# Kernel tuning notes

Measured on AMD Instinct MI355X. Metric: run time of the kernel, lower is better.

The kernel has to match this reference:

```python
import jax, jax.numpy as jnp
import numpy as np

B, N, T, D = 4, 256, 64, 128
DR, DH = 32, 128  # d_relation, d_hidden


def setup_inputs() -> dict:
    key = jax.random.key(0)
    ks = jax.random.split(key, 12)
    s = 0.05
    return {
        "H": jax.random.normal(ks[0], (B, N, T, D), jnp.float32),
        "R": jax.random.normal(ks[1], (B, N, N, DR), jnp.float32),
        "delta_H": jax.random.normal(ks[2], (B, N, T, D), jnp.float32),
        # params (torch Linear convention: W @ x + b with W shape (out, in))
        "Wq": jax.random.normal(ks[3], (DH, D), jnp.float32) * s,
        "bq": jnp.zeros((DH,), jnp.float32),
        "Wk": jax.random.normal(ks[4], (DH, D), jnp.float32) * s,
        "bk": jnp.zeros((DH,), jnp.float32),
        "Wr": jax.random.normal(ks[5], (DH, DR), jnp.float32) * s,
        "br": jnp.zeros((DH,), jnp.float32),
        "Wf": jax.random.normal(ks[6], (D, 3 * D + DR), jnp.float32) * s,
        "bf": jnp.zeros((D,), jnp.float32),
        "gamma": jnp.ones((D,), jnp.float32),
        "beta": jnp.zeros((D,), jnp.float32),
    }


def reference(H, R, delta_H, Wq, bq, Wk, bk, Wr, br, Wf, bf, gamma, beta):
    Bm, Nn, Tt, Dd = H.shape
    dr = R.shape[-1]

    # projections (eval mode: dropout is identity)
    q = jnp.einsum('bitd,hd->bith', H, Wq) + bq           # (B,N,T,DH)
    k = jnp.einsum('bjtd,hd->bjth', H, Wk) + bk           # (B,N,T,DH)
    rproj = jnp.einsum('bijr,hr->bijh', R, Wr) + br       # (B,N,N,DH)

    # attn_score[b,i,j,t] = <q_i[t], k_j[t] + Wr(r_ij)> / sqrt(d_model)
    scores = (jnp.einsum('bith,bjth->bijt', q, k)
              + jnp.einsum('bith,bijh->bijt', q, rproj)) / jnp.sqrt(jnp.asarray(Dd, H.dtype))
    w = jax.nn.softmax(scores, axis=-1)                   # softmax over time t
    # exclude the j == i pair (original loop skips it)
    w = w * (1.0 - jnp.eye(Nn, dtype=w.dtype))[None, :, :, None]

    # fuse Linear decomposed over the concat [h_i, h_j, r_ij, sum_t delta_h_j]
    W1 = Wf[:, :Dd]                 # acts on h_i
    W2 = Wf[:, Dd:2 * Dd]           # acts on h_j
    W3 = Wf[:, 2 * Dd:2 * Dd + dr]  # acts on r_ij
    W4 = Wf[:, 2 * Dd + dr:]        # acts on delta sum

    A = jnp.einsum('bitd,ed->bite', H, W1)                       # (B,N,T,D)
    Bj = jnp.einsum('bjtd,ed->bjte', H, W2)                      # (B,N,T,D)
    Cij = jnp.einsum('bijr,er->bije', R, W3)                     # (B,N,N,D)
    Ej = jnp.einsum('bjd,ed->bje', delta_H.sum(axis=2), W4)      # (B,N,D)

    wsum = w.sum(axis=2)                                         # (B,N,T)
    z = ((A + bf) * wsum[..., None]
         + jnp.einsum('bijt,bjte->bite', w, Bj)
         + jnp.einsum('bijt,bije->bite', w, Cij)
         + jnp.einsum('bijt,bje->bite', w, Ej))

    # residual + LayerNorm over last dim
    x = H + z
    mu = x.mean(axis=-1, keepdims=True)
    var = x.var(axis=-1, keepdims=True)
    return (x - mu) / jnp.sqrt(var + 1e-5) * gamma + beta
```

## Files before the change

kernel.cpp:

```cpp
#include <hip/hip_runtime.h>

typedef __attribute__((ext_vector_type(4))) float f32x4;
typedef __attribute__((ext_vector_type(8))) short short8;

constexpr int NB = 4, NS = 256, NT = 64, ND = 128, NR = 32;
constexpr int WFR = 3 * ND + NR;
constexpr float SCALE = 0.08838834764831845f;

__device__ __forceinline__ unsigned short f2bf(float f) {
  unsigned x = __float_as_uint(f);
  return (unsigned short)((x + 0x7FFFu + ((x >> 16) & 1u)) >> 16);
}
__device__ __forceinline__ float bf2f(unsigned short u) {
  return __uint_as_float((unsigned)u << 16);
}

__global__ __launch_bounds__(256) void kPrep(
    const float* __restrict__ Wq, const float* __restrict__ Wk,
    const float* __restrict__ Wr, const float* __restrict__ br,
    const float* __restrict__ bq, const float* __restrict__ Wf,
    const float* __restrict__ dH, const float* __restrict__ R,
    unsigned short* __restrict__ Wqb, unsigned short* __restrict__ Wkb,
    unsigned short* __restrict__ W1b, unsigned short* __restrict__ W2b,
    unsigned short* __restrict__ W3b, unsigned short* __restrict__ Wqrt,
    float* __restrict__ Gbias, unsigned short* __restrict__ Ejt,
    unsigned short* __restrict__ Rb, unsigned short* __restrict__ Rtb) {
  __shared__ __align__(16) char smem[17408];
  const int blk = blockIdx.x, tid = threadIdx.x;
  if (blk < 116) {
    if (blk < 64) {
      const int which = blk >> 4;
      const int idx = ((blk & 15) * 256 + tid) * 4;
      const int e = idx >> 7, d = idx & 127;
      float4 v;
      unsigned short* dst;
      if (which == 0)      { v = *(const float4*)&Wq[idx];            dst = Wqb; }
      else if (which == 1) { v = *(const float4*)&Wk[idx];            dst = Wkb; }
      else if (which == 2) { v = *(const float4*)&Wf[e * WFR + d];        dst = W1b; }
      else                 { v = *(const float4*)&Wf[e * WFR + ND + d];   dst = W2b; }
      dst[idx + 0] = f2bf(v.x); dst[idx + 1] = f2bf(v.y);
      dst[idx + 2] = f2bf(v.z); dst[idx + 3] = f2bf(v.w);
    } else if (blk < 68) {
      const int idx = ((blk - 64) * 256 + tid) * 4;
      const int e = idx >> 5, r = idx & 31;
      float4 v = *(const float4*)&Wf[e * WFR + 2 * ND + r];
      W3b[idx + 0] = f2bf(v.x); W3b[idx + 1] = f2bf(v.y);
      W3b[idx + 2] = f2bf(v.z); W3b[idx + 3] = f2bf(v.w);
    } else {
      const int rr = blk - 68;
      float* Vl = (float*)smem;
      float* gbl = Vl + 128;
      if (tid < 128) {
        float v = 0.f;
        if (rr < 32) v = Wr[tid * 32 + rr];
        else if (rr == 32) v = br[tid];
        Vl[tid] = v;
        gbl[tid] = bq[tid] * v;
      }
      __syncthreads();
      if (tid < 128) {
        float acc = 0.f;
        #pragma unroll 8
        for (int h = 0; h < 128; ++h) acc += Wq[h * 128 + tid] * Vl[h];
        Wqrt[rr * 128 + tid] = f2bf(acc * SCALE);
      }
      if (tid == 0) {
        float g = 0.f;
        for (int h = 0; h < 128; ++h) g += gbl[h];
        Gbias[rr] = g * SCALE;
      }
    }
  } else if (blk < 628) {
    float* ds = (float*)smem;
    const int half = tid >> 7, d = tid & 127;
    const int bj = (blk - 116) * 2 + half;
    const int b = bj >> 8, j = bj & 255;
    const float* p = dH + (size_t)bj * NT * ND + d;
    float s = 0.f;
    #pragma unroll 8
    for (int t = 0; t < NT; ++t) s += p[t * ND];
    ds[half * 128 + d] = s;
    __syncthreads();
    const float* w4 = Wf + (size_t)d * WFR + 2 * ND + NR;
    float acc = 0.f;
    #pragma unroll 8
    for (int dd = 0; dd < ND; ++dd) acc += ds[half * 128 + dd] * w4[dd];
    Ejt[((size_t)b * 128 + d) * 256 + j] = f2bf(acc);
  } else {
    unsigned short* rt = (unsigned short*)smem;
    const int bi = blk - 628;
    const float* src = R + (size_t)bi * 8192;
    #pragma unroll
    for (int it = 0; it < 8; ++it) {
      const int idx = (tid + it * 256) * 4;
      const float4 v = *(const float4*)&src[idx];
      const unsigned short s0 = f2bf(v.x), s1 = f2bf(v.y);
      const unsigned short s2 = f2bf(v.z), s3 = f2bf(v.w);
      unsigned long long p = (unsigned long long)s0 | ((unsigned long long)s1 << 16)
                           | ((unsigned long long)s2 << 32) | ((unsigned long long)s3 << 48);
      *(unsigned long long*)&Rb[(size_t)bi * 8192 + idx] = p;
      const int j = idx >> 5, r = idx & 31;
      *(unsigned*)&rt[j * 34 + r]     = (unsigned)s0 | ((unsigned)s1 << 16);
      *(unsigned*)&rt[j * 34 + r + 2] = (unsigned)s2 | ((unsigned)s3 << 16);
    }
    __syncthreads();
    #pragma unroll
    for (int it = 0; it < 4; ++it) {
      const int flat = (tid + it * 256) * 8;
      const int r = flat >> 8, j0 = flat & 255;
      short8 o;
      #pragma unroll
      for (int u = 0; u < 8; ++u) o[u] = (short)rt[(j0 + u) * 34 + r];
      *(short8*)&Rtb[(size_t)bi * 8192 + flat] = o;
    }
  }
}

__device__ __forceinline__ void gemm_tile(const short8 (&afr)[4][4],
    const unsigned short* __restrict__ Wp, int nt, int l15, int l4,
    f32x4 (&acc)[4]) {
  #pragma unroll
  for (int mt = 0; mt < 4; ++mt) acc[mt] = (f32x4){0.f, 0.f, 0.f, 0.f};
  #pragma unroll
  for (int kt = 0; kt < 4; ++kt) {
    short8 bfr = *(const short8*)(Wp + (16 * nt + l15) * 128 + 32 * kt + 8 * l4);
    #pragma unroll
    for (int mt = 0; mt < 4; ++mt)
      acc[mt] = __builtin_amdgcn_mfma_f32_16x16x32_bf16(afr[mt][kt], bfr, acc[mt], 0, 0, 0);
  }
}

__device__ __forceinline__ void gemm_tile2(const short8 (&afr)[2][4],
    const unsigned short* __restrict__ Wp, int nt, int l15, int l4,
    f32x4 (&acc)[2]) {
  #pragma unroll
  for (int mt = 0; mt < 2; ++mt) acc[mt] = (f32x4){0.f, 0.f, 0.f, 0.f};
  #pragma unroll
  for (int kt = 0; kt < 4; ++kt) {
    short8 bfr = *(const short8*)(Wp + (16 * nt + l15) * 128 + 32 * kt + 8 * l4);
    #pragma unroll
    for (int mt = 0; mt < 2; ++mt)
      acc[mt] = __builtin_amdgcn_mfma_f32_16x16x32_bf16(afr[mt][kt], bfr, acc[mt], 0, 0, 0);
  }
}

__global__ __launch_bounds__(256) void kB(const float* __restrict__ H,
    const unsigned short* __restrict__ W1b, const unsigned short* __restrict__ Wqrt,
    const float* __restrict__ Gbias, const float* __restrict__ bf,
    unsigned short* __restrict__ Apbb, unsigned short* __restrict__ Gb,
    unsigned short* __restrict__ Ht) {
  __shared__ unsigned short st[2][64 * 136];
  const int bn = blockIdx.x, tid = threadIdx.x;
  const int b = bn >> 8, n = bn & 255;
  const int lane = tid & 63, wv = tid >> 6;
  const int l15 = lane & 15, l4 = lane >> 4;
  short8 afr[4][4];
  const float* hb = H + (size_t)bn * (NT * ND);
  #pragma unroll
  for (int mt = 0; mt < 4; ++mt)
    #pragma unroll
    for (int kt = 0; kt < 4; ++kt) {
      const float* p = hb + (16 * mt + l15) * ND + 32 * kt + 8 * l4;
      float4 u0 = *(const float4*)p;
      float4 u1 = *(const float4*)(p + 4);
      short8 f;
      f[0] = (short)f2bf(u0.x); f[1] = (short)f2bf(u0.y);
      f[2] = (short)f2bf(u0.z); f[3] = (short)f2bf(u0.w);
      f[4] = (short)f2bf(u1.x); f[5] = (short)f2bf(u1.y);
      f[6] = (short)f2bf(u1.z); f[7] = (short)f2bf(u1.w);
      afr[mt][kt] = f;
    }
  f32x4 acc[4];
  #pragma unroll
  for (int n2 = 0; n2 < 2; ++n2) {
    const int nt = 2 * wv + n2, c = 16 * nt + l15;
    gemm_tile(afr, W1b, nt, l15, l4, acc);
    const float bias = bf[c];
    #pragma unroll
    for (int mt = 0; mt < 4; ++mt)
      #pragma unroll
      for (int jr = 0; jr < 4; ++jr)
        st[0][(16 * mt + 4 * l4 + jr) * 136 + c] = f2bf(acc[mt][jr] + bias);
  }
  if (wv < 3) {
    const int nt = wv, c = 16 * nt + l15;
    gemm_tile(afr, Wqrt, nt, l15, l4, acc);
    const float bias = Gbias[c];
    #pragma unroll
    for (int mt = 0; mt < 4; ++mt)
      #pragma unroll
      for (int jr = 0; jr < 4; ++jr) {
        const int tr = 16 * mt + 4 * l4 + jr;
        Gb[(size_t)bn * 3072 + tr * 48 + c] = f2bf(acc[mt][jr] + bias);
      }
  }
  if (wv == 0) {
    #pragma unroll
    for (int mt = 0; mt < 4; ++mt)
      #pragma unroll
      for (int kt = 0; kt < 4; ++kt)
        *(short8*)&st[1][(16 * mt + l15) * 136 + 32 * kt + 8 * l4] = afr[mt][kt];
  }
  __syncthreads();
  #pragma unroll
  for (int it = 0; it < 4; ++it) {
    const int flat = tid * 8 + it * 2048;
    const int row = flat >> 7, col = flat & 127;
    *(short8*)&Apbb[(size_t)bn * 8192 + flat] = *(const short8*)&st[0][row * 136 + col];
    *(short8*)&Ht[((size_t)(b * 64 + row) * 256 + n) * 128 + col] =
        *(const short8*)&st[1][row * 136 + col];
  }
}

__global__ __launch_bounds__(512) void kQK(const unsigned short* __restrict__ Ht,
    const unsigned short* __restrict__ Wqb, const unsigned short* __restrict__ Wkb,
    const float* __restrict__ bq, const float* __restrict__ bk,
    unsigned short* __restrict__ Sb) {
  __shared__ unsigned short qs[256 * 136];
  __shared__ unsigned short ks[256 * 136];
  const int bt = blockIdx.x;
  const int tid = threadIdx.x, lane = tid & 63, wv = tid >> 6;
  const int l15 = lane & 15, l4 = lane >> 4;
  const unsigned short* hsrc = Ht + (size_t)bt * (256 * 128);
  short8 afr[2][4];
  #pragma unroll
  for (int mt = 0; mt < 2; ++mt)
    #pragma unroll
    for (int kt = 0; kt < 4; ++kt) {
      const int n = 32 * wv + 16 * mt + l15;
      afr[mt][kt] = *(const short8*)(hsrc + n * 128 + 32 * kt + 8 * l4);
    }
  f32x4 acc[2];
  #pragma unroll 1
  for (int pass = 0; pass < 2; ++pass) {
    const unsigned short* W = (pass == 0) ? Wqb : Wkb;
    const float* bp = (pass == 0) ? bq : bk;
    unsigned short* dst = (pass == 0) ? qs : ks;
    #pragma unroll
    for (int nt = 0; nt < 8; ++nt) {
      gemm_tile2(afr, W, nt, l15, l4, acc);
      const int c = 16 * nt + l15;
      const float bias = bp[c];
      #pragma unroll
      for (int mt = 0; mt < 2; ++mt)
        #pragma unroll
        for (int jr = 0; jr < 4; ++jr)
          dst[(32 * wv + 16 * mt + 4 * l4 + jr) * 136 + c] = f2bf(acc[mt][jr] + bias);
    }
  }
  __syncthreads();
  short8 qa[2][4];
  #pragma unroll
  for (int mt = 0; mt < 2; ++mt)
    #pragma unroll
    for (int kt = 0; kt < 4; ++kt)
      qa[mt][kt] = *(const short8*)&qs[(32 * wv + 16 * mt + l15) * 136 + 32 * kt + 8 * l4];
  unsigned short* buf = qs + wv * (32 * 136);
  #pragma unroll 1
  for (int jh = 0; jh < 2; ++jh) {
    f32x4 sacc[2][8];
    #pragma unroll
    for (int mi = 0; mi < 2; ++mi)
      #pragma unroll
      for (int ntj = 0; ntj < 8; ++ntj) sacc[mi][ntj] = (f32x4){0.f, 0.f, 0.f, 0.f};
    #pragma unroll
    for (int kt = 0; kt < 4; ++kt) {
      short8 bb[8];
      #pragma unroll
      for (int ntj = 0; ntj < 8; ++ntj)
        bb[ntj] = *(const short8*)&ks[(16 * (8 * jh + ntj) + l15) * 136 + 32 * kt + 8 * l4];
      #pragma unroll
      for (int mi = 0; mi < 2; ++mi)
        #pragma unroll
        for (int ntj = 0; ntj < 8; ++ntj)
          sacc[mi][ntj] = __builtin_amdgcn_mfma_f32_16x16x32_bf16(qa[mi][kt], bb[ntj], sacc[mi][ntj], 0, 0, 0);
    }
    #pragma unroll
    for (int mi = 0; mi < 2; ++mi)
      #pragma unroll
      for (int ntj = 0; ntj < 8; ++ntj)
        #pragma unroll
        for (int jr = 0; jr < 4; ++jr)
          buf[(16 * mi + 4 * l4 + jr) * 136 + 16 * ntj + l15] =
              f2bf(sacc[mi][ntj][jr] * SCALE);
    #pragma unroll
    for (int it = 0; it < 8; ++it) {
      const int flat = lane * 8 + it * 512;
      const int row = flat >> 7, col = flat & 127;
      *(short8*)&Sb[((size_t)bt * 256 + 32 * wv + row) * 256 + 128 * jh + col] =
          *(const short8*)&buf[row * 136 + col];
    }
  }
}

__global__ __launch_bounds__(256) void kSM(
    const unsigned short* __restrict__ Gb, const unsigned short* __restrict__ Rb,
    const unsigned short* __restrict__ Rtb, const unsigned short* __restrict__ Sb,
    const unsigned short* __restrict__ W3b, const unsigned short* __restrict__ Apbb,
    unsigned short* __restrict__ Zt, unsigned short* __restrict__ Wbw) {
  __shared__ unsigned short wl[64 * 264];
  __shared__ unsigned short Ml[4][16 * 40];
  __shared__ float wred[4][64];
  __shared__ float wsl[64];
  const int bi = blockIdx.x, b = bi >> 8, i = bi & 255;
  const int tid = threadIdx.x, lane = tid & 63, wv = tid >> 6;
  const int l15 = lane & 15, l4 = lane >> 4;
  const f32x4 zz = (f32x4){0.f, 0.f, 0.f, 0.f};

  #pragma unroll
  for (int it = 0; it < 8; ++it) {
    const int flat = tid * 8 + it * 2048;
    const int t = flat >> 8, col = flat & 255;
    *(short8*)&wl[t * 264 + col] =
        *(const short8*)&Sb[(((size_t)b * 64 + t) * 256 + i) * 256 + col];
  }

  short8 ga[4];
  #pragma unroll
  for (int mt = 0; mt < 4; ++mt)
    ga[mt] = *(const short8*)(Gb + ((size_t)bi * 64 + 16 * mt + l15) * 48 + 8 * l4);
  f32x4 acc[4][4];
  #pragma unroll
  for (int nt = 0; nt < 4; ++nt) {
    const int j = 64 * wv + 16 * nt + l15;
    short8 rb = *(const short8*)(Rb + ((size_t)bi * 256 + j) * 32 + 8 * l4);
    #pragma unroll
    for (int mt = 0; mt < 4; ++mt)
      acc[mt][nt] = __builtin_amdgcn_mfma_f32_16x16x32_bf16(ga[mt], rb, zz, 0, 0, 0);
  }
  float qbr[4][4];
  #pragma unroll
  for (int mt = 0; mt < 4; ++mt)
    #pragma unroll
    for (int jr = 0; jr < 4; ++jr)
      qbr[mt][jr] = bf2f(Gb[((size_t)bi * 64 + 16 * mt + 4 * l4 + jr) * 48 + 32]);

  __syncthreads();

  #pragma unroll
  for (int mt = 0; mt < 4; ++mt)
    #pragma unroll
    for (int nt = 0; nt < 4; ++nt)
      #pragma unroll
      for (int jr = 0; jr < 4; ++jr)
        acc[mt][nt][jr] += bf2f(wl[(16 * mt + 4 * l4 + jr) * 264 + 64 * wv + 16 * nt + l15])
                         + qbr[mt][jr];

  #pragma unroll
  for (int nt = 0; nt < 4; ++nt) {
    float mx = -1e30f;
    #pragma unroll
    for (int mt = 0; mt < 4; ++mt)
      #pragma unroll
      for (int jr = 0; jr < 4; ++jr) mx = fmaxf(mx, acc[mt][nt][jr]);
    mx = fmaxf(mx, __shfl_xor(mx, 16));
    mx = fmaxf(mx, __shfl_xor(mx, 32));
    float sm = 0.f;
    #pragma unroll
    for (int mt = 0; mt < 4; ++mt)
      #pragma unroll
      for (int jr = 0; jr < 4; ++jr) {
        const float e = __expf(acc[mt][nt][jr] - mx);
        acc[mt][nt][jr] = e;
        sm += e;
      }
    sm += __shfl_xor(sm, 16);
    sm += __shfl_xor(sm, 32);
    const int j = 64 * wv + 16 * nt + l15;
    const float inv = (j == i) ? 0.f : 1.f / sm;
    #pragma unroll
    for (int mt = 0; mt < 4; ++mt)
      #pragma unroll
      for (int jr = 0; jr < 4; ++jr) acc[mt][nt][jr] *= inv;
  }

  float part[4][4];
  #pragma unroll
  for (int mt = 0; mt < 4; ++mt)
    #pragma unroll
    for (int jr = 0; jr < 4; ++jr) {
      float s = 0.f;
      #pragma unroll
      for (int nt = 0; nt < 4; ++nt) s += acc[mt][nt][jr];
      part[mt][jr] = s;
    }
  #pragma unroll
  for (int m = 1; m < 16; m <<= 1)
    #pragma unroll
    for (int mt = 0; mt < 4; ++mt)
      #pragma unroll
      for (int jr = 0; jr < 4; ++jr) part[mt][jr] += __shfl_xor(part[mt][jr], m);
  if (l15 == 0) {
    #pragma unroll
    for (int mt = 0; mt < 4; ++mt)
      #pragma unroll
      for (int jr = 0; jr < 4; ++jr) wred[wv][16 * mt + 4 * l4 + jr] = part[mt][jr];
  }

  #pragma unroll
  for (int mt = 0; mt < 4; ++mt)
    #pragma unroll
    for (int nt = 0; nt < 4; ++nt)
      #pragma unroll
      for (int jr = 0; jr < 4; ++jr)
        wl[(16 * mt + 4 * l4 + jr) * 264 + 64 * wv + 16 * nt + l15] =
            f2bf(acc[mt][nt][jr]);

  __syncthreads();

  if (tid < 64) wsl[tid] = wred[0][tid] + wred[1][tid] + wred[2][tid] + wred[3][tid];

  #pragma unroll
  for (int it = 0; it < 8; ++it) {
    const int flat = tid * 8 + it * 2048;
    const int t = flat >> 8, j = flat & 255;
    *(short8*)&Wbw[(((size_t)(b * 64 + t)) * 256 + i) * 256 + j] =
        *(const short8*)&wl[t * 264 + j];
  }

  f32x4 mac[2];
  mac[0] = zz; mac[1] = zz;
  #pragma unroll
  for (int kt = 0; kt < 8; ++kt) {
    short8 a = *(const short8*)&wl[(16 * wv + l15) * 264 + 32 * kt + 8 * l4];
    #pragma unroll
    for (int nt = 0; nt < 2; ++nt) {
      short8 bb = *(const short8*)(Rtb + ((size_t)bi * 32 + 16 * nt + l15) * 256 + 32 * kt + 8 * l4);
      mac[nt] = __builtin_amdgcn_mfma_f32_16x16x32_bf16(a, bb, mac[nt], 0, 0, 0);
    }
  }
  #pragma unroll
  for (int nt = 0; nt < 2; ++nt)
    #pragma unroll
    for (int jr = 0; jr < 4; ++jr)
      Ml[wv][(4 * l4 + jr) * 40 + 16 * nt + l15] = f2bf(mac[nt][jr]);
  asm volatile("s_waitcnt lgkmcnt(0)" ::: "memory");
  short8 a2 = *(const short8*)&Ml[wv][l15 * 40 + 8 * l4];
  f32x4 tac[8];
  #pragma unroll
  for (int nt = 0; nt < 8; ++nt) {
    short8 w3 = *(const short8*)(W3b + (16 * nt + l15) * 32 + 8 * l4);
    tac[nt] = __builtin_amdgcn_mfma_f32_16x16x32_bf16(a2, w3, zz, 0, 0, 0);
  }
  __syncthreads();

  const size_t abase = (size_t)bi * 8192;
  #pragma unroll
  for (int it = 0; it < 4; ++it) {
    const int flat = tid * 8 + it * 2048;
    const int row = flat >> 7, col = flat & 127;
    *(short8*)&wl[row * 136 + col] = *(const short8*)&Apbb[abase + flat];
  }
  __syncthreads();
  #pragma unroll
  for (int jr = 0; jr < 4; ++jr) {
    const int t = 16 * wv + 4 * l4 + jr;
    const float ws = wsl[t];
    #pragma unroll
    for (int nt = 0; nt < 8; ++nt) {
      const int e = 16 * nt + l15;
      const int off = t * 136 + e;
      wl[off] = f2bf(bf2f(wl[off]) * ws + tac[nt][jr]);
    }
  }
  __syncthreads();
  #pragma unroll
  for (int it = 0; it < 4; ++it) {
    const int flat = tid * 8 + it * 2048;
    const int row = flat >> 7, col = flat & 127;
    *(short8*)&Zt[((size_t)(b * 64 + row) * 256 + i) * 128 + col] =
        *(const short8*)&wl[row * 136 + col];
  }
}

__global__ __launch_bounds__(512) void kD(const unsigned short* __restrict__ Wb,
    const unsigned short* __restrict__ Ht, const unsigned short* __restrict__ W2b,
    const unsigned short* __restrict__ Ejt, const unsigned short* __restrict__ Zt,
    const float* __restrict__ gamma, const float* __restrict__ beta,
    float* __restrict__ out) {
  __shared__ unsigned short Bl[128 * 264];
  const int bt = blockIdx.x;
  const int b = bt >> 6, t = bt & 63;
  const int tid = threadIdx.x, lane = tid & 63, wv = tid >> 6;
  const int l15 = lane & 15, l4 = lane >> 4;
  {
    const unsigned short* esrc = Ejt + (size_t)b * (128 * 256);
    #pragma unroll
    for (int it = 0; it < 8; ++it) {
      const int flat = tid * 8 + it * 4096;
      const int e = flat >> 8, j = flat & 255;
      *(short8*)&Bl[e * 264 + j] = *(const short8*)&esrc[flat];
    }
  }
  const unsigned short* hsrc = Ht + (size_t)bt * (256 * 128);
  short8 hfr[2][4];
  #pragma unroll
  for (int mt = 0; mt < 2; ++mt)
    #pragma unroll
    for (int kt = 0; kt < 4; ++kt) {
      const int j = 32 * wv + 16 * mt + l15;
      hfr[mt][kt] = *(const short8*)(hsrc + j * 128 + 32 * kt + 8 * l4);
    }
  __syncthreads();
  #pragma unroll
  for (int nt = 0; nt < 8; ++nt) {
    f32x4 be[2];
    be[0] = (f32x4){0.f, 0.f, 0.f, 0.f};
    be[1] = (f32x4){0.f, 0.f, 0.f, 0.f};
    #pragma unroll
    for (int kt = 0; kt < 4; ++kt) {
      short8 w2 = *(const short8*)(W2b + (16 * nt + l15) * 128 + 32 * kt + 8 * l4);
      #pragma unroll
      for (int mt = 0; mt < 2; ++mt)
        be[mt] = __builtin_amdgcn_mfma_f32_16x16x32_bf16(hfr[mt][kt], w2, be[mt], 0, 0, 0);
    }
    #pragma unroll
    for (int mt = 0; mt < 2; ++mt)
      #pragma unroll
      for (int jr = 0; jr < 4; ++jr) {
        const int idx = (16 * nt + l15) * 264 + 32 * wv + 16 * mt + 4 * l4 + jr;
        Bl[idx] = f2bf(be[mt][jr] + bf2f(Bl[idx]));
      }
  }
  __syncthreads();
  f32x4 acc[2][8];
  #pragma unroll
  for (int m2 = 0; m2 < 2; ++m2)
    #pragma unroll
    for (int nt = 0; nt < 8; ++nt) acc[m2][nt] = (f32x4){0.f, 0.f, 0.f, 0.f};
  #pragma unroll
  for (int kt = 0; kt < 8; ++kt) {
    short8 a[2];
    #pragma unroll
    for (int m2 = 0; m2 < 2; ++m2) {
      const int i = 32 * wv + 16 * m2 + l15;
      a[m2] = *(const short8*)(Wb + ((size_t)(b * 64 + t) * 256 + i) * 256 + 32 * kt + 8 * l4);
    }
    #pragma unroll
    for (int nt = 0; nt < 8; ++nt) {
      short8 bb = *(const short8*)(&Bl[(16 * nt + l15) * 264 + 32 * kt + 8 * l4]);
      #pragma unroll
      for (int m2 = 0; m2 < 2; ++m2)
        acc[m2][nt] = __builtin_amdgcn_mfma_f32_16x16x32_bf16(a[m2], bb, acc[m2][nt], 0, 0, 0);
    }
  }
  unsigned short* Zl = Bl;
  #pragma unroll 1
  for (int src = 0; src < 2; ++src) {
    const unsigned short* gsrc = (src == 0) ? Zt : Ht;
    __syncthreads();
    #pragma unroll
    for (int it = 0; it < 8; ++it) {
      const int flat = tid * 8 + it * 4096;
      const int row = flat >> 7, col = flat & 127;
      *(short8*)&Zl[row * 132 + col] =
          *(const short8*)&gsrc[((size_t)bt * 256 + row) * 128 + col];
    }
    __syncthreads();
    #pragma unroll
    for (int m2 = 0; m2 < 2; ++m2)
      #pragma unroll
      for (int jr = 0; jr < 4; ++jr) {
        const int i = 32 * wv + 16 * m2 + 4 * l4 + jr;
        #pragma unroll
        for (int nt = 0; nt < 8; ++nt)
          acc[m2][nt][jr] += bf2f(Zl[i * 132 + 16 * nt + l15]);
      }
  }
  float gam[8], bet[8];
  #pragma unroll
  for (int nt = 0; nt < 8; ++nt) {
    const int e = 16 * nt + l15;
    gam[nt] = gamma[e];
    bet[nt] = beta[e];
  }
  #pragma unroll
  for (int m2 = 0; m2 < 2; ++m2)
    #pragma unroll
    for (int jr = 0; jr < 4; ++jr) {
      const int i = 32 * wv + 16 * m2 + 4 * l4 + jr;
      const size_t base = ((size_t)(b * 256 + i) * 64 + t) * 128;
      float sm = 0.f, sq = 0.f;
      #pragma unroll
      for (int nt = 0; nt < 8; ++nt) {
        const float v = acc[m2][nt][jr];
        sm += v;
        sq += v * v;
      }
      #pragma unroll
      for (int m = 1; m < 16; m <<= 1) {
        sm += __shfl_xor(sm, m);
        sq += __shfl_xor(sq, m);
      }
      const float mu = sm * (1.f / 128.f);
      const float inv = rsqrtf(sq * (1.f / 128.f) - mu * mu + 1e-5f);
      #pragma unroll
      for (int nt = 0; nt < 8; ++nt)
        out[base + 16 * nt + l15] = (acc[m2][nt][jr] - mu) * inv * gam[nt] + bet[nt];
    }
}

extern "C" void kernel_launch(void* const* d_in, const int* in_sizes, int n_in,
                              void* d_out, int out_size, void* d_ws, size_t ws_size,
                              hipStream_t stream) {
  (void)in_sizes; (void)n_in; (void)out_size; (void)ws_size;
  const float* H     = (const float*)d_in[0];
  const float* R     = (const float*)d_in[1];
  const float* dH    = (const float*)d_in[2];
  const float* Wq    = (const float*)d_in[3];
  const float* bq    = (const float*)d_in[4];
  const float* Wk    = (const float*)d_in[5];
  const float* bk    = (const float*)d_in[6];
  const float* Wr    = (const float*)d_in[7];
  const float* br    = (const float*)d_in[8];
  const float* Wf    = (const float*)d_in[9];
  const float* bf    = (const float*)d_in[10];
  const float* gamma = (const float*)d_in[11];
  const float* beta  = (const float*)d_in[12];
  float* out = (float*)d_out;
  char* w = (char*)d_ws;

  unsigned short* Wbw  = (unsigned short*)(w + 0);
  unsigned short* Sb   = (unsigned short*)(w + 33554432);
  unsigned short* Apbb = (unsigned short*)(w + 67108864);
  unsigned short* Gb   = (unsigned short*)(w + 83886080);
  unsigned short* Rb   = (unsigned short*)(w + 90177536);
  unsigned short* Rtb  = (unsigned short*)(w + 106954752);
  unsigned short* Ejt  = (unsigned short*)(w + 123731968);
  unsigned short* Wqb  = (unsigned short*)(w + 123994112);
  unsigned short* Wkb  = (unsigned short*)(w + 124026880);
  unsigned short* W1b  = (unsigned short*)(w + 124059648);
  unsigned short* W2b  = (unsigned short*)(w + 124092416);
  unsigned short* W3b  = (unsigned short*)(w + 124125184);
  unsigned short* Wqrt = (unsigned short*)(w + 124133376);
  float*          Gbs  = (float*)(w + 124145664);
  unsigned short* Ht   = (unsigned short*)(w + 124145856);
  unsigned short* Zt   = (unsigned short*)(w + 140923072);

  kPrep<<<dim3(1652), dim3(256), 0, stream>>>(Wq, Wk, Wr, br, bq, Wf, dH, R,
                                              Wqb, Wkb, W1b, W2b, W3b, Wqrt,
                                              Gbs, Ejt, Rb, Rtb);
  kB<<<dim3(NB * NS), dim3(256), 0, stream>>>(H, W1b, Wqrt, Gbs, bf,
                                              Apbb, Gb, Ht);
  kQK<<<dim3(NB * NT), dim3(512), 0, stream>>>(Ht, Wqb, Wkb, bq, bk, Sb);
  kSM<<<dim3(NB * NS), dim3(256), 0, stream>>>(Gb, Rb, Rtb, Sb, W3b,
                                               Apbb, Zt, Wbw);
  kD<<<dim3(NB * NT), dim3(512), 0, stream>>>(Wbw, Ht, W2b, Ejt, Zt,
                                              gamma, beta, out);
}
```

Before: 144.5 us.

## Split weight prep into a small kernel and merge data prep into kB

```diff
diff --git a/kernel.cpp b/kernel.cpp
--- a/kernel.cpp
+++ b/kernel.cpp
@@ -15,65 +15,164 @@
   return __uint_as_float((unsigned)u << 16);
 }
 
-__global__ __launch_bounds__(256) void kPrep(
+__global__ __launch_bounds__(256) void kPrepW(
     const float* __restrict__ Wq, const float* __restrict__ Wk,
     const float* __restrict__ Wr, const float* __restrict__ br,
     const float* __restrict__ bq, const float* __restrict__ Wf,
-    const float* __restrict__ dH, const float* __restrict__ R,
     unsigned short* __restrict__ Wqb, unsigned short* __restrict__ Wkb,
     unsigned short* __restrict__ W1b, unsigned short* __restrict__ W2b,
     unsigned short* __restrict__ W3b, unsigned short* __restrict__ Wqrt,
-    float* __restrict__ Gbias, unsigned short* __restrict__ Ejt,
+    float* __restrict__ Gbias) {
+  __shared__ float Vl[128];
+  __shared__ float gbl[128];
+  const int blk = blockIdx.x, tid = threadIdx.x;
+  if (blk < 64) {
+    const int which = blk >> 4;
+    const int idx = ((blk & 15) * 256 + tid) * 4;
+    const int e = idx >> 7, d = idx & 127;
+    float4 v;
+    unsigned short* dst;
+    if (which == 0)      { v = *(const float4*)&Wq[idx];            dst = Wqb; }
+    else if (which == 1) { v = *(const float4*)&Wk[idx];            dst = Wkb; }
+    else if (which == 2) { v = *(const float4*)&Wf[e * WFR + d];        dst = W1b; }
+    else                 { v = *(const float4*)&Wf[e * WFR + ND + d];   dst = W2b; }
+    dst[idx + 0] = f2bf(v.x); dst[idx + 1] = f2bf(v.y);
+    dst[idx + 2] = f2bf(v.z); dst[idx + 3] = f2bf(v.w);
+  } else if (blk < 68) {
+    const int idx = ((blk - 64) * 256 + tid) * 4;
+    const int e = idx >> 5, r = idx & 31;
+    float4 v = *(const float4*)&Wf[e * WFR + 2 * ND + r];
+    W3b[idx + 0] = f2bf(v.x); W3b[idx + 1] = f2bf(v.y);
+    W3b[idx + 2] = f2bf(v.z); W3b[idx + 3] = f2bf(v.w);
+  } else {
+    const int rr = blk - 68;
+    if (tid < 128) {
+      float v = 0.f;
+      if (rr < 32) v = Wr[tid * 32 + rr];
+      else if (rr == 32) v = br[tid];
+      Vl[tid] = v;
+      gbl[tid] = bq[tid] * v;
+    }
+    __syncthreads();
+    if (tid < 128) {
+      float acc = 0.f;
+      #pragma unroll 8
+      for (int h = 0; h < 128; ++h) acc += Wq[h * 128 + tid] * Vl[h];
+      Wqrt[rr * 128 + tid] = f2bf(acc * SCALE);
+    }
+    if (tid == 0) {
+      float g = 0.f;
+      for (int h = 0; h < 128; ++h) g += gbl[h];
+      Gbias[rr] = g * SCALE;
+    }
+  }
+}
+
+__device__ __forceinline__ void gemm_tile(const short8 (&afr)[4][4],
+    const unsigned short* __restrict__ Wp, int nt, int l15, int l4,
+    f32x4 (&acc)[4]) {
+  #pragma unroll
+  for (int mt = 0; mt < 4; ++mt) acc[mt] = (f32x4){0.f, 0.f, 0.f, 0.f};
+  #pragma unroll
+  for (int kt = 0; kt < 4; ++kt) {
+    short8 bfr = *(const short8*)(Wp + (16 * nt + l15) * 128 + 32 * kt + 8 * l4);
+    #pragma unroll
+    for (int mt = 0; mt < 4; ++mt)
+      acc[mt] = __builtin_amdgcn_mfma_f32_16x16x32_bf16(afr[mt][kt], bfr, acc[mt], 0, 0, 0);
+  }
+}
+
+__device__ __forceinline__ void gemm_tile2(const short8 (&afr)[2][4],
+    const unsigned short* __restrict__ Wp, int nt, int l15, int l4,
+    f32x4 (&acc)[2]) {
+  #pragma unroll
+  for (int mt = 0; mt < 2; ++mt) acc[mt] = (f32x4){0.f, 0.f, 0.f, 0.f};
+  #pragma unroll
+  for (int kt = 0; kt < 4; ++kt) {
+    short8 bfr = *(const short8*)(Wp + (16 * nt + l15) * 128 + 32 * kt + 8 * l4);
+    #pragma unroll
+    for (int mt = 0; mt < 2; ++mt)
+      acc[mt] = __builtin_amdgcn_mfma_f32_16x16x32_bf16(afr[mt][kt], bfr, acc[mt], 0, 0, 0);
+  }
+}
+
+__global__ __launch_bounds__(256) void kB2(const float* __restrict__ H,
+    const unsigned short* __restrict__ W1b, const unsigned short* __restrict__ Wqrt,
+    const float* __restrict__ Gbias, const float* __restrict__ bf,
+    const float* __restrict__ dH, const float* __restrict__ Wf,
+    const float* __restrict__ R,
+    unsigned short* __restrict__ Apbb, unsigned short* __restrict__ Gb,
+    unsigned short* __restrict__ Ht, unsigned short* __restrict__ Ejt,
     unsigned short* __restrict__ Rb, unsigned short* __restrict__ Rtb) {
-  __shared__ __align__(16) char smem[17408];
+  __shared__ __align__(16) char smem[34816];
   const int blk = blockIdx.x, tid = threadIdx.x;
-  if (blk < 116) {
-    if (blk < 64) {
-      const int which = blk >> 4;
-      const int idx = ((blk & 15) * 256 + tid) * 4;
-      const int e = idx >> 7, d = idx & 127;
-      float4 v;
-      unsigned short* dst;
-      if (which == 0)      { v = *(const float4*)&Wq[idx];            dst = Wqb; }
-      else if (which == 1) { v = *(const float4*)&Wk[idx];            dst = Wkb; }
-      else if (which == 2) { v = *(const float4*)&Wf[e * WFR + d];        dst = W1b; }
-      else                 { v = *(const float4*)&Wf[e * WFR + ND + d];   dst = W2b; }
-      dst[idx + 0] = f2bf(v.x); dst[idx + 1] = f2bf(v.y);
-      dst[idx + 2] = f2bf(v.z); dst[idx + 3] = f2bf(v.w);
-    } else if (blk < 68) {
-      const int idx = ((blk - 64) * 256 + tid) * 4;
-      const int e = idx >> 5, r = idx & 31;
-      float4 v = *(const float4*)&Wf[e * WFR + 2 * ND + r];
-      W3b[idx + 0] = f2bf(v.x); W3b[idx + 1] = f2bf(v.y);
-      W3b[idx + 2] = f2bf(v.z); W3b[idx + 3] = f2bf(v.w);
-    } else {
-      const int rr = blk - 68;
-      float* Vl = (float*)smem;
-      float* gbl = Vl + 128;
-      if (tid < 128) {
-        float v = 0.f;
-        if (rr < 32) v = Wr[tid * 32 + rr];
-        else if (rr == 32) v = br[tid];
-        Vl[tid] = v;
-        gbl[tid] = bq[tid] * v;
+  if (blk < 1024) {
+    unsigned short* st0 = (unsigned short*)smem;
+    unsigned short* st1 = (unsigned short*)smem + 64 * 136;
+    const int bn = blk;
+    const int b = bn >> 8, n = bn & 255;
+    const int lane = tid & 63, wv = tid >> 6;
+    const int l15 = lane & 15, l4 = lane >> 4;
+    short8 afr[4][4];
+    const float* hb = H + (size_t)bn * (NT * ND);
+    #pragma unroll
+    for (int mt = 0; mt < 4; ++mt)
+      #pragma unroll
+      for (int kt = 0; kt < 4; ++kt) {
+        const float* p = hb + (16 * mt + l15) * ND + 32 * kt + 8 * l4;
+        float4 u0 = *(const float4*)p;
+        float4 u1 = *(const float4*)(p + 4);
+        short8 f;
+        f[0] = (short)f2bf(u0.x); f[1] = (short)f2bf(u0.y);
+        f[2] = (short)f2bf(u0.z); f[3] = (short)f2bf(u0.w);
+        f[4] = (short)f2bf(u1.x); f[5] = (short)f2bf(u1.y);
+        f[6] = (short)f2bf(u1.z); f[7] = (short)f2bf(u1.w);
+        afr[mt][kt] = f;
       }
-      __syncthreads();
-      if (tid < 128) {
-        float acc = 0.f;
-        #pragma unroll 8
-        for (int h = 0; h < 128; ++h) acc += Wq[h * 128 + tid] * Vl[h];
-        Wqrt[rr * 128 + tid] = f2bf(acc * SCALE);
-      }
-      if (tid == 0) {
-        float g = 0.f;
-        for (int h = 0; h < 128; ++h) g += gbl[h];
-        Gbias[rr] = g * SCALE;
-      }
-    }
-  } else if (blk < 628) {
+    f32x4 acc[4];
+    #pragma unroll
+    for (int n2 = 0; n2 < 2; ++n2) {
+      const int nt = 2 * wv + n2, c = 16 * nt + l15;
+      gemm_tile(afr, W1b, nt, l15, l4, acc);
+      const float bias = bf[c];
+      #pragma unroll
+      for (int mt = 0; mt < 4; ++mt)
+        #pragma unroll
+        for (int jr = 0; jr < 4; ++jr)
+          st0[(16 * mt + 4 * l4 + jr) * 136 + c] = f2bf(acc[mt][jr] + bias);
+    }
+    if (wv < 3) {
+      const int nt = wv, c = 16 * nt + l15;
+      gemm_tile(afr, Wqrt, nt, l15, l4, acc);
+      const float bias = Gbias[c];
+      #pragma unroll
+      for (int mt = 0; mt < 4; ++mt)
+        #pragma unroll
+        for (int jr = 0; jr < 4; ++jr) {
+          const int tr = 16 * mt + 4 * l4 + jr;
+          Gb[(size_t)bn * 3072 + tr * 48 + c] = f2bf(acc[mt][jr] + bias);
+        }
+    }
+    if (wv == 0) {
+      #pragma unroll
+      for (int mt = 0; mt < 4; ++mt)
+        #pragma unroll
+        for (int kt = 0; kt < 4; ++kt)
+          *(short8*)&st1[(16 * mt + l15) * 136 + 32 * kt + 8 * l4] = afr[mt][kt];
+    }
+    __syncthreads();
+    #pragma unroll
+    for (int it = 0; it < 4; ++it) {
+      const int flat = tid * 8 + it * 2048;
+      const int row = flat >> 7, col = flat & 127;
+      *(short8*)&Apbb[(size_t)bn * 8192 + flat] = *(const short8*)&st0[row * 136 + col];
+      *(short8*)&Ht[((size_t)(b * 64 + row) * 256 + n) * 128 + col] =
+          *(const short8*)&st1[row * 136 + col];
+    }
+  } else if (blk < 1536) {
     float* ds = (float*)smem;
     const int half = tid >> 7, d = tid & 127;
-    const int bj = (blk - 116) * 2 + half;
+    const int bj = (blk - 1024) * 2 + half;
     const int b = bj >> 8, j = bj & 255;
     const float* p = dH + (size_t)bj * NT * ND + d;
     float s = 0.f;
@@ -88,7 +187,7 @@
     Ejt[((size_t)b * 128 + d) * 256 + j] = f2bf(acc);
   } else {
     unsigned short* rt = (unsigned short*)smem;
-    const int bi = blk - 628;
+    const int bi = blk - 1536;
     const float* src = R + (size_t)bi * 8192;
     #pragma unroll
     for (int it = 0; it < 8; ++it) {
@@ -113,102 +212,6 @@
       for (int u = 0; u < 8; ++u) o[u] = (short)rt[(j0 + u) * 34 + r];
       *(short8*)&Rtb[(size_t)bi * 8192 + flat] = o;
     }
-  }
-}
-
-__device__ __forceinline__ void gemm_tile(const short8 (&afr)[4][4],
-    const unsigned short* __restrict__ Wp, int nt, int l15, int l4,
-    f32x4 (&acc)[4]) {
-  #pragma unroll
-  for (int mt = 0; mt < 4; ++mt) acc[mt] = (f32x4){0.f, 0.f, 0.f, 0.f};
-  #pragma unroll
-  for (int kt = 0; kt < 4; ++kt) {
-    short8 bfr = *(const short8*)(Wp + (16 * nt + l15) * 128 + 32 * kt + 8 * l4);
-    #pragma unroll
-    for (int mt = 0; mt < 4; ++mt)
-      acc[mt] = __builtin_amdgcn_mfma_f32_16x16x32_bf16(afr[mt][kt], bfr, acc[mt], 0, 0, 0);
-  }
-}
-
-__device__ __forceinline__ void gemm_tile2(const short8 (&afr)[2][4],
-    const unsigned short* __restrict__ Wp, int nt, int l15, int l4,
-    f32x4 (&acc)[2]) {
-  #pragma unroll
-  for (int mt = 0; mt < 2; ++mt) acc[mt] = (f32x4){0.f, 0.f, 0.f, 0.f};
-  #pragma unroll
-  for (int kt = 0; kt < 4; ++kt) {
-    short8 bfr = *(const short8*)(Wp + (16 * nt + l15) * 128 + 32 * kt + 8 * l4);
-    #pragma unroll
-    for (int mt = 0; mt < 2; ++mt)
-      acc[mt] = __builtin_amdgcn_mfma_f32_16x16x32_bf16(afr[mt][kt], bfr, acc[mt], 0, 0, 0);
-  }
-}
-
-__global__ __launch_bounds__(256) void kB(const float* __restrict__ H,
-    const unsigned short* __restrict__ W1b, const unsigned short* __restrict__ Wqrt,
-    const float* __restrict__ Gbias, const float* __restrict__ bf,
-    unsigned short* __restrict__ Apbb, unsigned short* __restrict__ Gb,
-    unsigned short* __restrict__ Ht) {
-  __shared__ unsigned short st[2][64 * 136];
-  const int bn = blockIdx.x, tid = threadIdx.x;
-  const int b = bn >> 8, n = bn & 255;
-  const int lane = tid & 63, wv = tid >> 6;
-  const int l15 = lane & 15, l4 = lane >> 4;
-  short8 afr[4][4];
-  const float* hb = H + (size_t)bn * (NT * ND);
-  #pragma unroll
-  for (int mt = 0; mt < 4; ++mt)
-    #pragma unroll
-    for (int kt = 0; kt < 4; ++kt) {
-      const float* p = hb + (16 * mt + l15) * ND + 32 * kt + 8 * l4;
-      float4 u0 = *(const float4*)p;
-      float4 u1 = *(const float4*)(p + 4);
-      short8 f;
-      f[0] = (short)f2bf(u0.x); f[1] = (short)f2bf(u0.y);
-      f[2] = (short)f2bf(u0.z); f[3] = (short)f2bf(u0.w);
-      f[4] = (short)f2bf(u1.x); f[5] = (short)f2bf(u1.y);
-      f[6] = (short)f2bf(u1.z); f[7] = (short)f2bf(u1.w);
-      afr[mt][kt] = f;
-    }
-  f32x4 acc[4];
-  #pragma unroll
-  for (int n2 = 0; n2 < 2; ++n2) {
-    const int nt = 2 * wv + n2, c = 16 * nt + l15;
-    gemm_tile(afr, W1b, nt, l15, l4, acc);
-    const float bias = bf[c];
-    #pragma unroll
-    for (int mt = 0; mt < 4; ++mt)
-      #pragma unroll
-      for (int jr = 0; jr < 4; ++jr)
-        st[0][(16 * mt + 4 * l4 + jr) * 136 + c] = f2bf(acc[mt][jr] + bias);
-  }
-  if (wv < 3) {
-    const int nt = wv, c = 16 * nt + l15;
-    gemm_tile(afr, Wqrt, nt, l15, l4, acc);
-    const float bias = Gbias[c];
-    #pragma unroll
-    for (int mt = 0; mt < 4; ++mt)
-      #pragma unroll
-      for (int jr = 0; jr < 4; ++jr) {
-        const int tr = 16 * mt + 4 * l4 + jr;
-        Gb[(size_t)bn * 3072 + tr * 48 + c] = f2bf(acc[mt][jr] + bias);
-      }
-  }
-  if (wv == 0) {
-    #pragma unroll
-    for (int mt = 0; mt < 4; ++mt)
-      #pragma unroll
-      for (int kt = 0; kt < 4; ++kt)
-        *(short8*)&st[1][(16 * mt + l15) * 136 + 32 * kt + 8 * l4] = afr[mt][kt];
-  }
-  __syncthreads();
-  #pragma unroll
-  for (int it = 0; it < 4; ++it) {
-    const int flat = tid * 8 + it * 2048;
-    const int row = flat >> 7, col = flat & 127;
-    *(short8*)&Apbb[(size_t)bn * 8192 + flat] = *(const short8*)&st[0][row * 136 + col];
-    *(short8*)&Ht[((size_t)(b * 64 + row) * 256 + n) * 128 + col] =
-        *(const short8*)&st[1][row * 136 + col];
   }
 }
 
@@ -637,11 +640,10 @@
   unsigned short* Ht   = (unsigned short*)(w + 124145856);
   unsigned short* Zt   = (unsigned short*)(w + 140923072);
 
-  kPrep<<<dim3(1652), dim3(256), 0, stream>>>(Wq, Wk, Wr, br, bq, Wf, dH, R,
-                                              Wqb, Wkb, W1b, W2b, W3b, Wqrt,
-                                              Gbs, Ejt, Rb, Rtb);
-  kB<<<dim3(NB * NS), dim3(256), 0, stream>>>(H, W1b, Wqrt, Gbs, bf,
-                                              Apbb, Gb, Ht);
+  kPrepW<<<dim3(116), dim3(256), 0, stream>>>(Wq, Wk, Wr, br, bq, Wf,
+                                              Wqb, Wkb, W1b, W2b, W3b, Wqrt, Gbs);
+  kB2<<<dim3(2560), dim3(256), 0, stream>>>(H, W1b, Wqrt, Gbs, bf, dH, Wf, R,
+                                            Apbb, Gb, Ht, Ejt, Rb, Rtb);
   kQK<<<dim3(NB * NT), dim3(512), 0, stream>>>(Ht, Wqb, Wkb, bq, bk, Sb);
   kSM<<<dim3(NB * NS), dim3(256), 0, stream>>>(Gb, Rb, Rtb, Sb, W3b,
                                                Apbb, Zt, Wbw);
```

New measurement: 153.0 us. 1.06x slower.
